# Kernel optimization log

Measured on AMD Instinct MI355X. Metric: run time of the kernel, lower is better.

Reference implementation:

```python
import jax, jax.numpy as jnp
import numpy as np

EPS = 0.01  # diffusion sampling noise scale


def gru_last(x, Wx, Wh, bx, bh):
    """Run a single-layer GRU (torch gate conventions) over x: [B, L, C] -> final hidden [B, H]."""
    B, L, C = x.shape
    H = Wh.shape[0]
    xg = jnp.einsum('blc,cg->blg', x, Wx) + bx  # precomputed input gates [B, L, 3H]

    def step(h, xg_t):
        hg = h @ Wh + bh
        xr, xz, xn = jnp.split(xg_t, 3, axis=-1)
        hr, hz, hn = jnp.split(hg, 3, axis=-1)
        r = jax.nn.sigmoid(xr + hr)
        z = jax.nn.sigmoid(xz + hz)
        n = jnp.tanh(xn + r * hn)
        h_new = (1.0 - z) * n + z * h
        return h_new, None

    h0 = jnp.zeros((B, H), x.dtype)
    h, _ = jax.lax.scan(step, h0, jnp.swapaxes(xg, 0, 1))
    return h


def gru_aggr(x, Wx, Wh, bx, bh, Wo, bo):
    return gru_last(x, Wx, Wh, bx, bh) @ Wo + bo


def setup_inputs() -> dict:
    key = jax.random.key(0)
    N, C, DEG, H, C_OUT, T = 8000, 64, 16, 128, 64, 4
    ks = jax.random.split(key, 16)

    def lin(k, fan_in, shape):
        return jax.random.normal(k, shape, dtype=jnp.float32) / np.sqrt(fan_in)

    inp = {
        'node_attr': jax.random.normal(ks[0], (N, C), dtype=jnp.float32),
        'neighbors': jax.random.randint(ks[1], (N, DEG), 0, N, dtype=jnp.int32),
        'noise': jax.random.normal(ks[2], (T, N, DEG), dtype=jnp.float32),
        # diff_aggr GRU + output head (edge log-prob comes from channel 0)
        'dWx': lin(ks[3], C, (C, 3 * H)),
        'dWh': lin(ks[4], H, (H, 3 * H)),
        'dbx': jnp.zeros((3 * H,), jnp.float32),
        'dbh': jnp.zeros((3 * H,), jnp.float32),
        'dWo': lin(ks[5], H, (H, C_OUT)),
        'dbo': jnp.zeros((C_OUT,), jnp.float32),
        # walk_aggr GRU + output head (node embedding)
        'wWx': lin(ks[6], C, (C, 3 * H)),
        'wWh': lin(ks[7], H, (H, 3 * H)),
        'wbx': jnp.zeros((3 * H,), jnp.float32),
        'wbh': jnp.zeros((3 * H,), jnp.float32),
        'wWo': lin(ks[8], H, (H, C_OUT)),
        'wbo': jnp.zeros((C_OUT,), jnp.float32),
    }
    return inp


def reference(node_attr, neighbors, noise,
              dWx, dWh, dbx, dbh, dWo, dbo,
              wWx, wWh, wbx, wbh, wWo, wbo):
    N, C = node_attr.shape
    DEG = neighbors.shape[1]
    T = noise.shape[0]

    cur = jnp.arange(N)                      # current frontier of each walk
    walk_embeds = node_attr[:, None, :]      # [N, L, C], L grows each step
    logps = []
    for t in range(T):
        nbr = neighbors[cur]                 # [N, DEG] candidate next hops
        cand = node_attr[nbr]                # [N, DEG, C]
        L = walk_embeds.shape[1]
        prefix = jnp.broadcast_to(walk_embeds[:, None], (N, DEG, L, C))
        seq = jnp.concatenate([prefix, cand[:, :, None, :]], axis=2)  # [N, DEG, L+1, C]
        seq = seq.reshape(N * DEG, L + 1, C)
        logp = gru_aggr(seq, dWx, dWh, dbx, dbh, dWo, dbo)[:, 0].reshape(N, DEG)
        # per-source-node log-softmax normalizer (no_grad in original)
        norm = jax.lax.stop_gradient(jax.nn.logsumexp(logp, axis=1, keepdims=True))
        logp = logp - norm
        p = jnp.exp(logp)
        noisy = p + EPS * noise[t]
        sel = jnp.argmax(noisy, axis=1)      # scatter_max over each node's candidates
        logps.append(jnp.take_along_axis(logp, sel[:, None], axis=1)[:, 0])
        cur = jnp.take_along_axis(nbr, sel[:, None], axis=1)[:, 0]
        walk_embeds = jnp.concatenate([walk_embeds, node_attr[cur][:, None, :]], axis=1)

    walks_logp = jnp.stack(logps, axis=1)    # [N, T]
    v_out = gru_aggr(walk_embeds, wWx, wWh, wbx, wbh, wWo, wbo)  # [N, C_OUT]
    return v_out, walks_logp
```

## Files before the change

kernel.cpp:

```cpp
#include <hip/hip_runtime.h>
#include <math.h>

#define NN 8000
#define CD 64
#define DG 16
#define HD 128
#define G3 384
#define TT 4
#define MARGIN 4e-3f

#if __has_builtin(__builtin_amdgcn_rcpf)
#define RCP(x) __builtin_amdgcn_rcpf(x)
#else
#define RCP(x) (1.f/(x))
#endif

__device__ __forceinline__ float fsig (float x){ return RCP(1.f + __expf(-x)); }
__device__ __forceinline__ float ftanh(float x){ return 1.f - 2.f*RCP(1.f + __expf(2.f*x)); }

__device__ __forceinline__ double fexp64(double x){
    const double LOG2E  = 1.4426950408889634074;
    const double LN2_HI = 6.93147180369123816490e-01;
    const double LN2_LO = 1.90821492927058770002e-10;
    x = fmin(fmax(x, -700.0), 700.0);
    double fn = rint(x * LOG2E);
    double r  = fma(-fn, LN2_HI, x);
    r = fma(-fn, LN2_LO, r);
    double p = 1.6059043836821613e-10;
    p = fma(p, r, 2.0876756987868099e-09);
    p = fma(p, r, 2.5052108385441719e-08);
    p = fma(p, r, 2.7557319223985893e-07);
    p = fma(p, r, 2.7557319223985888e-06);
    p = fma(p, r, 2.4801587301587302e-05);
    p = fma(p, r, 1.9841269841269841e-04);
    p = fma(p, r, 1.3888888888888889e-03);
    p = fma(p, r, 8.3333333333333332e-03);
    p = fma(p, r, 4.1666666666666664e-02);
    p = fma(p, r, 1.6666666666666666e-01);
    p = fma(p, r, 0.5);
    p = fma(p, r, 1.0);
    p = fma(p, r, 1.0);
    long long bits = __double_as_longlong(p) + ((long long)(int)fn << 52);
    return __longlong_as_double(bits);
}
__device__ __forceinline__ double sig64f (double x){ return 1.0/(1.0 + fexp64(-x)); }
__device__ __forceinline__ double tanh64f(double x){ return 1.0 - 2.0/(fexp64(2.0*x) + 1.0); }

__global__ __launch_bounds__(384) void xg_kernel(const float* __restrict__ A,
    const float* __restrict__ W, const float* __restrict__ b,
    float* __restrict__ hiP, float* __restrict__ loP)
{
    __shared__ float a_s[8][64];
    const int g  = threadIdx.x;
    const int l  = g & 63, q = g >> 6;
    const int n0 = blockIdx.x * 8;
    for (int idx = threadIdx.x; idx < 8*64; idx += 384)
        a_s[idx>>6][idx&63] = A[(size_t)n0*64 + idx];
    __syncthreads();
    double acc[8];
    const double bg = (double)b[g];
#pragma unroll
    for (int j=0;j<8;j++) acc[j] = bg;
    for (int c=0;c<64;c++){
        const double w = (double)W[c*G3 + g];
#pragma unroll
        for (int j=0;j<8;j++) acc[j] += (double)a_s[j][c]*w;
    }
#pragma unroll
    for (int j=0;j<8;j++){
        const size_t base = (size_t)(n0+j)*64 + l;
        const float hi = (float)acc[j];
        hiP[base*8 + q] = hi;
        if (q < 2) hiP[base*8 + 6 + q] = 0.f;
        if (loP) loP[base*6 + q] = (float)(acc[j] - (double)hi);
    }
}

__global__ __launch_bounds__(256) void repack_kernel(const float* __restrict__ W,
                                                     float* __restrict__ P)
{
    const int idx = blockIdx.x*256 + threadIdx.x;
    const int k = idx >> 9, rem = idx & 511, l = rem >> 3, s = rem & 7;
    P[idx] = (s < 6) ? W[k*G3 + s*64 + l] : 0.f;
}

__global__ __launch_bounds__(256) void walk_kernel(
    const int*   __restrict__ nbrs,  const float* __restrict__ noise,
    const float* __restrict__ XGfP,  const float* __restrict__ dWhP,
    const float* __restrict__ dbh,   const float* __restrict__ dWo,
    const float* __restrict__ dbo,
    int* __restrict__ paths, int* __restrict__ fail_cnt, int* __restrict__ fail_list,
    float* __restrict__ out)
{
    __shared__ float hf_s[4][HD];
    __shared__ float part_s[4][4][6][64];

    const int wid  = threadIdx.x >> 6;
    const int lane = threadIdx.x & 63;
    const int node = blockIdx.x*4 + wid;

    float h0 = 0.f, h1 = 0.f;
    float dbhf[6], hgf[6];
#pragma unroll
    for (int m=0;m<6;m++){ dbhf[m] = dbh[lane+64*m]; hgf[m] = dbhf[m]; }
    const float wo0f0 = dWo[lane*CD];
    const float wo0f1 = dWo[(lane+64)*CD];
    const float dbo0f = dbo[0];

    int cur = node;
    int ch0=0, ch1=0, ch2=0, ch3=0;
    int tripmask = 0;

    for (int t=0;t<TT;t++){
        if      (t==0) ch0 = cur;
        else if (t==1) ch1 = cur;
        else if (t==2) ch2 = cur;
        else           ch3 = cur;

        {
            const float4* xr = (const float4*)(XGfP + ((size_t)cur*64 + lane)*8);
            const float4 A = xr[0], B = xr[1];
            float r = fsig (A.x + hgf[0]);
            float z = fsig (A.z + hgf[2]);
            float n = ftanh(B.x + r*hgf[4]);
            h0 = (1.f-z)*n + z*h0;
            r = fsig (A.y + hgf[1]);
            z = fsig (A.w + hgf[3]);
            n = ftanh(B.y + r*hgf[5]);
            h1 = (1.f-z)*n + z*h1;
        }
        hf_s[wid][lane] = h0;  hf_s[wid][lane+64] = h1;
        __syncthreads();

        {
            float pacc[4][6];
#pragma unroll
            for (int j=0;j<4;j++)
#pragma unroll
                for (int m=0;m<6;m++) pacc[j][m] = 0.f;
            const float4* wr = (const float4*)(dWhP + (size_t)lane*8);
#pragma unroll 4
            for (int kk=0; kk<32; kk++){
                const int k = wid*32 + kk;
                const float4 W0 = wr[k*128], W1 = wr[k*128+1];
#pragma unroll
                for (int j=0;j<4;j++){
                    const float hk = hf_s[j][k];
                    pacc[j][0] += hk*W0.x; pacc[j][1] += hk*W0.y;
                    pacc[j][2] += hk*W0.z; pacc[j][3] += hk*W0.w;
                    pacc[j][4] += hk*W1.x; pacc[j][5] += hk*W1.y;
                }
            }
#pragma unroll
            for (int j=0;j<4;j++)
#pragma unroll
                for (int m=0;m<6;m++) part_s[wid][j][m][lane] = pacc[j][m];
        }
        __syncthreads();

#pragma unroll
        for (int m=0;m<6;m++)
            hgf[m] = dbhf[m] + part_s[0][wid][m][lane] + part_s[1][wid][m][lane]
                             + part_s[2][wid][m][lane] + part_s[3][wid][m][lane];

        int   nbrv = (lane < DG) ? nbrs[(size_t)cur*DG + lane] : 0;
        float nz   = (lane < DG) ? noise[((size_t)t*NN + node)*DG + lane] : 0.f;
        float lf = -3.0e38f;
#pragma unroll
        for (int g=0; g<4; g++){
            float4 CA[4], CB[4];
#pragma unroll
            for (int j=0;j<4;j++){
                const int nd = __shfl(nbrv, g*4+j);
                const float4* cr = (const float4*)(XGfP + ((size_t)nd*64 + lane)*8);
                CA[j] = cr[0];  CB[j] = cr[1];
            }
            float part[4];
#pragma unroll
            for (int j=0;j<4;j++){
                float r = fsig (CA[j].x + hgf[0]);
                float z = fsig (CA[j].z + hgf[2]);
                float n = ftanh(CB[j].x + r*hgf[4]);
                part[j]  = ((1.f-z)*n + z*h0) * wo0f0;
                r = fsig (CA[j].y + hgf[1]);
                z = fsig (CA[j].w + hgf[3]);
                n = ftanh(CB[j].y + r*hgf[5]);
                part[j] += ((1.f-z)*n + z*h1) * wo0f1;
            }
#pragma unroll
            for (int off=32; off>0; off>>=1){
#pragma unroll
                for (int j=0;j<4;j++) part[j] += __shfl_xor(part[j], off);
            }
#pragma unroll
            for (int j=0;j<4;j++) if (lane == g*4+j) lf = part[j] + dbo0f;
        }

        float v  = (lane < DG) ? lf : -3.0e38f;
        float mx = v;
#pragma unroll
        for (int off=32; off>0; off>>=1) mx = fmaxf(mx, __shfl_xor(mx, off));
        float e = (lane < DG) ? __expf(v - mx) : 0.f;
        float s = e;
#pragma unroll
        for (int off=32; off>0; off>>=1) s += __shfl_xor(s, off);
        const float normf = mx + __logf(s);

        float noisyf = (lane < DG) ? __expf(v - normf) + 0.01f*nz : -3.0e38f;
        int   idx = lane;
        float bv  = noisyf;
#pragma unroll
        for (int off=32; off>0; off>>=1){
            float ov = __shfl_xor(bv, off);
            int   oi = __shfl_xor(idx, off);
            if (ov > bv || (ov == bv && oi < idx)){ bv = ov; idx = oi; }
        }
        float sv = (lane == idx || lane >= DG) ? -3.0e38f : noisyf;
#pragma unroll
        for (int off=32; off>0; off>>=1) sv = fmaxf(sv, __shfl_xor(sv, off));

        if ((bv - sv) < MARGIN) tripmask |= (1 << t);

        const float lpf = __shfl(v, idx) - normf;
        if (lane == 0) out[NN*CD + node*TT + t] = lpf;
        cur = __shfl(nbrv, idx);
    }

    if (lane == 0){
        int* p = paths + (size_t)node*8;
        p[0]=ch0; p[1]=ch1; p[2]=ch2; p[3]=ch3; p[4]=cur;
        if (tripmask){
            const int bin = 31 - __clz(tripmask);
            const int slot = atomicAdd(&fail_cnt[bin], 1);
            fail_list[bin*NN + slot] = node | (tripmask << 16);
        }
    }
}

__global__ __launch_bounds__(256) void fix_kernel(
    const int*   __restrict__ nbrs,  const float* __restrict__ noise,
    const float* __restrict__ XGfP,  const float* __restrict__ XGrP,
    const float* __restrict__ dWhP,  const float* __restrict__ dbh,
    const float* __restrict__ dWo,   const float* __restrict__ dbo,
    const int* __restrict__ fail_cnt, const int* __restrict__ fail_list,
    int* __restrict__ paths, float* __restrict__ out)
{
    __shared__ double smem[3584];
    double* h_s  = smem;
    double* dbuf = smem + 512;

    const int wid  = threadIdx.x >> 6;
    const int lane = threadIdx.x & 63;
    const int n0c = fail_cnt[0], n1c = fail_cnt[1], n2c = fail_cnt[2], n3c = fail_cnt[3];
    const int total = n0c + n1c + n2c + n3c;
    if (blockIdx.x*4 >= total) return;

    const int  ii     = blockIdx.x*4 + wid;
    const bool active = (ii < total);
    int entry = 0;
    if (active){
        int b, loc;
        if      (ii < n0c)            { b=0; loc=ii; }
        else if (ii < n0c+n1c)        { b=1; loc=ii-n0c; }
        else if (ii < n0c+n1c+n2c)    { b=2; loc=ii-n0c-n1c; }
        else                          { b=3; loc=ii-n0c-n1c-n2c; }
        entry = fail_list[b*NN + loc];
    }
    const int  node = entry & 0xFFFF;
    const int  mask = active ? (entry >> 16) : 0;
    const int* pw   = paths + (size_t)node*8;

    double db64[6];
#pragma unroll
    for (int m=0;m<6;m++) db64[m] = (double)dbh[lane+64*m];
    const double wo0d0 = (double)dWo[lane*CD];
    const double wo0d1 = (double)dWo[(lane+64)*CD];
    const double dbo0d = (double)dbo[0];

    double H0 = 0.0, H1 = 0.0;
    double g64[6];
#pragma unroll
    for (int m=0;m<6;m++) g64[m] = db64[m];
    int  cur = node;
    int  c0=0,c1=0,c2=0,c3=0;
    bool diverged = false;

    for (int t=0;t<TT;t++){
        const bool done = !diverged && ((mask >> t) == 0);
        if (__syncthreads_and(done ? 1 : 0)) break;

        if      (t==0) c0 = cur;
        else if (t==1) c1 = cur;
        else if (t==2) c2 = cur;
        else           c3 = cur;

        if (!done){
            const size_t b = (size_t)cur*64 + lane;
            const float* hi = XGfP + b*8;
            const float* lo = XGrP + b*6;
            double r = sig64f (((double)hi[0]+(double)lo[0]) + g64[0]);
            double z = sig64f (((double)hi[2]+(double)lo[2]) + g64[2]);
            double n = tanh64f(((double)hi[4]+(double)lo[4]) + r*g64[4]);
            H0 = (1.0-z)*n + z*H0;
            r = sig64f (((double)hi[1]+(double)lo[1]) + g64[1]);
            z = sig64f (((double)hi[3]+(double)lo[3]) + g64[3]);
            n = tanh64f(((double)hi[5]+(double)lo[5]) + r*g64[5]);
            H1 = (1.0-z)*n + z*H1;
            h_s[wid*HD + lane] = H0;  h_s[wid*HD + lane + 64] = H1;
        }
        __syncthreads();

        double pacc[4][6];
#pragma unroll
        for (int j=0;j<4;j++)
#pragma unroll
            for (int m=0;m<6;m++) pacc[j][m] = 0.0;
        {
            const float4* wv = (const float4*)(dWhP + (size_t)lane*8);
#pragma unroll 4
            for (int kk=0; kk<32; kk++){
                const int k = wid*32 + kk;
                const float4 W0 = wv[k*128], W1 = wv[k*128+1];
#pragma unroll
                for (int j=0;j<4;j++){
                    const double hk = h_s[j*HD + k];
                    pacc[j][0] += hk*(double)W0.x; pacc[j][1] += hk*(double)W0.y;
                    pacc[j][2] += hk*(double)W0.z; pacc[j][3] += hk*(double)W0.w;
                    pacc[j][4] += hk*(double)W1.x; pacc[j][5] += hk*(double)W1.y;
                }
            }
        }
        if (wid >= 2){
#pragma unroll
            for (int j=0;j<4;j++)
#pragma unroll
                for (int m=0;m<6;m++)
                    dbuf[(((wid-2)*4+j)*6+m)*64 + lane] = pacc[j][m];
        }
        __syncthreads();
        if (wid < 2){
#pragma unroll
            for (int j=0;j<4;j++)
#pragma unroll
                for (int m=0;m<6;m++){
                    pacc[j][m] += dbuf[((wid*4+j)*6+m)*64 + lane];
                    dbuf[((wid*4+j)*6+m)*64 + lane] = pacc[j][m];
                }
        }
        __syncthreads();
        if (!done){
#pragma unroll
            for (int m=0;m<6;m++)
                g64[m] = db64[m] + dbuf[((0*4+wid)*6+m)*64 + lane]
                                 + dbuf[((1*4+wid)*6+m)*64 + lane];
        }

        if (!diverged && !((mask >> t) & 1)){
            cur = pw[t+1];
            continue;
        }

        int   nbrv = (lane < DG) ? nbrs[(size_t)cur*DG + lane] : 0;
        float nz   = (lane < DG) ? noise[((size_t)t*NN + node)*DG + lane] : 0.f;
        double lv = -1e300;
#pragma unroll
        for (int g=0; g<4; g++){
            float ch[4][6], cl[4][6];
#pragma unroll
            for (int j=0;j<4;j++){
                const int nd = __shfl(nbrv, g*4+j);
                const size_t b = (size_t)nd*64 + lane;
                const float* hi = XGfP + b*8;
                const float* lo = XGrP + b*6;
#pragma unroll
                for (int q=0;q<6;q++){ ch[j][q]=hi[q]; cl[j][q]=lo[q]; }
            }
#pragma unroll
            for (int j=0;j<4;j++){
                double r = sig64f (((double)ch[j][0]+(double)cl[j][0]) + g64[0]);
                double z = sig64f (((double)ch[j][2]+(double)cl[j][2]) + g64[2]);
                double n = tanh64f(((double)ch[j][4]+(double)cl[j][4]) + r*g64[4]);
                double part = ((1.0-z)*n + z*H0) * wo0d0;
                r = sig64f (((double)ch[j][1]+(double)cl[j][1]) + g64[1]);
                z = sig64f (((double)ch[j][3]+(double)cl[j][3]) + g64[3]);
                n = tanh64f(((double)ch[j][5]+(double)cl[j][5]) + r*g64[5]);
                part += ((1.0-z)*n + z*H1) * wo0d1;
#pragma unroll
                for (int off=32; off>0; off>>=1) part += __shfl_xor(part, off);
                if (lane == g*4+j) lv = part + dbo0d;
            }
        }

        double dv = (lane < DG) ? lv : -1e300;
        double dmx = dv;
#pragma unroll
        for (int off=32; off>0; off>>=1) dmx = fmax(dmx, __shfl_xor(dmx, off));
        double de = (lane < DG) ? fexp64(dv - dmx) : 0.0;
        double ds = de;
#pragma unroll
        for (int off=32; off>0; off>>=1) ds += __shfl_xor(ds, off);
        const double dnorm = dmx + log(ds);
        double dnoisy = (lane < DG) ? fexp64(dv - dnorm) + 0.01*(double)nz : -1e300;
        int di = lane;
#pragma unroll
        for (int off=32; off>0; off>>=1){
            double ov = __shfl_xor(dnoisy, off);
            int    oi = __shfl_xor(di, off);
            if (ov > dnoisy || (ov == dnoisy && oi < di)){ dnoisy = ov; di = oi; }
        }
        const double lpfix = __shfl(dv, di) - dnorm;
        if (active && lane == 0) out[NN*CD + node*TT + t] = (float)lpfix;
        const int newcur = __shfl(nbrv, di);
        diverged = diverged || (newcur != pw[t+1]);
        cur = newcur;
    }

    if (active && diverged && lane == 0){
        int* p = paths + (size_t)node*8;
        p[0]=c0; p[1]=c1; p[2]=c2; p[3]=c3; p[4]=cur;
    }
}

__global__ __launch_bounds__(256) void wgru_kernel(
    const int*   __restrict__ paths, const float* __restrict__ XGwP,
    const float* __restrict__ wWhP,  const float* __restrict__ wbh,
    const float* __restrict__ wWo,   const float* __restrict__ wbo,
    float* __restrict__ out)
{
    __shared__ float hw_s[4][HD];
    __shared__ float part_s[4][4][6][64];
    const int wid  = threadIdx.x >> 6;
    const int lane = threadIdx.x & 63;
    const int node = blockIdx.x*4 + wid;

    float h0 = 0.f, h1 = 0.f;
    float wb[6], hg[6];
#pragma unroll
    for (int m=0;m<6;m++){ wb[m] = wbh[lane+64*m]; hg[m] = wb[m]; }
    const int* p = paths + (size_t)node*8;

#pragma unroll
    for (int s=0; s<=TT; s++){
        const int c = p[s];
        const float4* xr = (const float4*)(XGwP + ((size_t)c*64 + lane)*8);
        const float4 A = xr[0], B = xr[1];
        float r = fsig (A.x + hg[0]);
        float z = fsig (A.z + hg[2]);
        float n = ftanh(B.x + r*hg[4]);
        h0 = (1.f-z)*n + z*h0;
        r = fsig (A.y + hg[1]);
        z = fsig (A.w + hg[3]);
        n = ftanh(B.y + r*hg[5]);
        h1 = (1.f-z)*n + z*h1;
        if (s < TT){
            hw_s[wid][lane] = h0;  hw_s[wid][lane+64] = h1;
            __syncthreads();
            float pacc[4][6];
#pragma unroll
            for (int j=0;j<4;j++)
#pragma unroll
                for (int m=0;m<6;m++) pacc[j][m] = 0.f;
            const float4* wr = (const float4*)(wWhP + (size_t)lane*8);
#pragma unroll 4
            for (int kk=0; kk<32; kk++){
                const int k = wid*32 + kk;
                const float4 W0 = wr[k*128], W1 = wr[k*128+1];
#pragma unroll
                for (int j=0;j<4;j++){
                    const float hk = hw_s[j][k];
                    pacc[j][0] += hk*W0.x; pacc[j][1] += hk*W0.y;
                    pacc[j][2] += hk*W0.z; pacc[j][3] += hk*W0.w;
                    pacc[j][4] += hk*W1.x; pacc[j][5] += hk*W1.y;
                }
            }
#pragma unroll
            for (int j=0;j<4;j++)
#pragma unroll
                for (int m=0;m<6;m++) part_s[wid][j][m][lane] = pacc[j][m];
            __syncthreads();
#pragma unroll
            for (int m=0;m<6;m++)
                hg[m] = wb[m] + part_s[0][wid][m][lane] + part_s[1][wid][m][lane]
                              + part_s[2][wid][m][lane] + part_s[3][wid][m][lane];
        }
    }
    hw_s[wid][lane] = h0;  hw_s[wid][lane+64] = h1;
    __syncthreads();

    float acc = wbo[lane];
    const float* wcol = wWo + lane;
    for (int i=0;i<HD;i++) acc += hw_s[wid][i] * wcol[(size_t)i*CD];
    out[(size_t)node*CD + lane] = acc;
}

extern "C" void kernel_launch(void* const* d_in, const int* in_sizes, int n_in,
                              void* d_out, int out_size, void* d_ws, size_t ws_size,
                              hipStream_t stream)
{
    const float* attr  = (const float*)d_in[0];
    const int*   nbrs  = (const int*)  d_in[1];
    const float* noise = (const float*)d_in[2];
    const float* dWx = (const float*)d_in[3];
    const float* dWh = (const float*)d_in[4];
    const float* dbx = (const float*)d_in[5];
    const float* dbh = (const float*)d_in[6];
    const float* dWo = (const float*)d_in[7];
    const float* dbo = (const float*)d_in[8];
    const float* wWx = (const float*)d_in[9];
    const float* wWh = (const float*)d_in[10];
    const float* wbx = (const float*)d_in[11];
    const float* wbh = (const float*)d_in[12];
    const float* wWo = (const float*)d_in[13];
    const float* wbo = (const float*)d_in[14];
    float* out = (float*)d_out;

    char* ws = (char*)d_ws;
    float* XGfP      = (float*)(ws);
    float* XGrP      = (float*)(ws + 16384000);
    float* XGwP      = (float*)(ws + 28672000);
    float* dWhP      = (float*)(ws + 45056000);
    float* wWhP      = (float*)(ws + 45318144);
    int*   paths     = (int*)  (ws + 45580288);
    int*   fail_list = (int*)  (ws + 45836288);
    int*   fail_cnt  = (int*)  (ws + 45964288);

    hipMemsetAsync(fail_cnt, 0, 4*sizeof(int), stream);

    xg_kernel<<<NN/8, G3, 0, stream>>>(attr, dWx, dbx, XGfP, XGrP);
    xg_kernel<<<NN/8, G3, 0, stream>>>(attr, wWx, wbx, XGwP, nullptr);
    repack_kernel<<<(HD*64*8)/256, 256, 0, stream>>>(dWh, dWhP);
    repack_kernel<<<(HD*64*8)/256, 256, 0, stream>>>(wWh, wWhP);

    walk_kernel<<<NN/4, 256, 0, stream>>>(nbrs, noise, XGfP, dWhP,
                                          dbh, dWo, dbo,
                                          paths, fail_cnt, fail_list, out);
    fix_kernel<<<2000, 256, 0, stream>>>(nbrs, noise, XGfP, XGrP,
                                         dWhP, dbh, dWo, dbo,
                                         fail_cnt, fail_list, paths, out);
    wgru_kernel<<<NN/4, 256, 0, stream>>>(paths, XGwP, wWhP, wbh, wWo, wbo, out);
}
```

Before: 492.9 us.

## Prefetch neighbor gate rows and tree-reduce hidden partials through smaller shared buffer

The walk kernel now issues the next step's input-gate row, neighbor list and noise loads right after the current step's selection. Candidate gate rows are double-buffered in groups of four, so loads for the next group overlap scoring of the current one, and the first group's loads start before the recurrent matvec. The cross-warp reduction of recurrent partials becomes a two-level reduction through a half-size shared buffer, in both the walk and walk-GRU kernels. In exchange there is an extra barrier per step and more live registers, which may lower occupancy.

```diff
diff --git a/kernel.cpp b/kernel.cpp
--- a/kernel.cpp
+++ b/kernel.cpp
@@ -93,7 +93,7 @@
     float* __restrict__ out)
 {
     __shared__ float hf_s[4][HD];
-    __shared__ float part_s[4][4][6][64];
+    __shared__ float dbuf_s[2][4][6][64];
 
     const int wid  = threadIdx.x >> 6;
     const int lane = threadIdx.x & 63;
@@ -110,6 +110,47 @@
     int cur = node;
     int ch0=0, ch1=0, ch2=0, ch3=0;
     int tripmask = 0;
+
+    float4 XA, XB; int nbrv; float nz;
+    {
+        const float4* xr = (const float4*)(XGfP + ((size_t)cur*64 + lane)*8);
+        XA = xr[0];  XB = xr[1];
+        nbrv = (lane < DG) ? nbrs[(size_t)cur*DG + lane] : 0;
+        nz   = (lane < DG) ? noise[(size_t)node*DG + lane] : 0.f;
+    }
+
+    float4 PA[4], PB[4], QA[4], QB[4];
+    float lf;
+
+    auto loadGroup = [&](float4* A, float4* B, int gbase){
+#pragma unroll
+        for (int j=0;j<4;j++){
+            const int nd = __shfl(nbrv, gbase+j);
+            const float4* cr = (const float4*)(XGfP + ((size_t)nd*64 + lane)*8);
+            A[j] = cr[0];  B[j] = cr[1];
+        }
+    };
+    auto scoreGroup = [&](const float4* A, const float4* B, int gbase){
+        float part[4];
+#pragma unroll
+        for (int j=0;j<4;j++){
+            float r = fsig (A[j].x + hgf[0]);
+            float z = fsig (A[j].z + hgf[2]);
+            float n = ftanh(B[j].x + r*hgf[4]);
+            part[j]  = ((1.f-z)*n + z*h0) * wo0f0;
+            r = fsig (A[j].y + hgf[1]);
+            z = fsig (A[j].w + hgf[3]);
+            n = ftanh(B[j].y + r*hgf[5]);
+            part[j] += ((1.f-z)*n + z*h1) * wo0f1;
+        }
+#pragma unroll
+        for (int off=32; off>0; off>>=1){
+#pragma unroll
+            for (int j=0;j<4;j++) part[j] += __shfl_xor(part[j], off);
+        }
+#pragma unroll
+        for (int j=0;j<4;j++) if (lane == gbase+j) lf = part[j] + dbo0f;
+    };
 
     for (int t=0;t<TT;t++){
         if      (t==0) ch0 = cur;
@@ -118,26 +159,26 @@
         else           ch3 = cur;
 
         {
-            const float4* xr = (const float4*)(XGfP + ((size_t)cur*64 + lane)*8);
-            const float4 A = xr[0], B = xr[1];
-            float r = fsig (A.x + hgf[0]);
-            float z = fsig (A.z + hgf[2]);
-            float n = ftanh(B.x + r*hgf[4]);
+            float r = fsig (XA.x + hgf[0]);
+            float z = fsig (XA.z + hgf[2]);
+            float n = ftanh(XB.x + r*hgf[4]);
             h0 = (1.f-z)*n + z*h0;
-            r = fsig (A.y + hgf[1]);
-            z = fsig (A.w + hgf[3]);
-            n = ftanh(B.y + r*hgf[5]);
+            r = fsig (XA.y + hgf[1]);
+            z = fsig (XA.w + hgf[3]);
+            n = ftanh(XB.y + r*hgf[5]);
             h1 = (1.f-z)*n + z*h1;
         }
         hf_s[wid][lane] = h0;  hf_s[wid][lane+64] = h1;
         __syncthreads();
 
+        loadGroup(PA, PB, 0);
+
+        float pacc[4][6];
+#pragma unroll
+        for (int j=0;j<4;j++)
+#pragma unroll
+            for (int m=0;m<6;m++) pacc[j][m] = 0.f;
         {
-            float pacc[4][6];
-#pragma unroll
-            for (int j=0;j<4;j++)
-#pragma unroll
-                for (int m=0;m<6;m++) pacc[j][m] = 0.f;
             const float4* wr = (const float4*)(dWhP + (size_t)lane*8);
 #pragma unroll 4
             for (int kk=0; kk<32; kk++){
@@ -151,50 +192,33 @@
                     pacc[j][4] += hk*W1.x; pacc[j][5] += hk*W1.y;
                 }
             }
+        }
+        if (wid >= 2){
 #pragma unroll
             for (int j=0;j<4;j++)
 #pragma unroll
-                for (int m=0;m<6;m++) part_s[wid][j][m][lane] = pacc[j][m];
+                for (int m=0;m<6;m++) dbuf_s[wid-2][j][m][lane] = pacc[j][m];
         }
         __syncthreads();
-
+        if (wid < 2){
+#pragma unroll
+            for (int j=0;j<4;j++)
+#pragma unroll
+                for (int m=0;m<6;m++){
+                    pacc[j][m] += dbuf_s[wid][j][m][lane];
+                    dbuf_s[wid][j][m][lane] = pacc[j][m];
+                }
+        }
+        __syncthreads();
 #pragma unroll
         for (int m=0;m<6;m++)
-            hgf[m] = dbhf[m] + part_s[0][wid][m][lane] + part_s[1][wid][m][lane]
-                             + part_s[2][wid][m][lane] + part_s[3][wid][m][lane];
-
-        int   nbrv = (lane < DG) ? nbrs[(size_t)cur*DG + lane] : 0;
-        float nz   = (lane < DG) ? noise[((size_t)t*NN + node)*DG + lane] : 0.f;
-        float lf = -3.0e38f;
-#pragma unroll
-        for (int g=0; g<4; g++){
-            float4 CA[4], CB[4];
-#pragma unroll
-            for (int j=0;j<4;j++){
-                const int nd = __shfl(nbrv, g*4+j);
-                const float4* cr = (const float4*)(XGfP + ((size_t)nd*64 + lane)*8);
-                CA[j] = cr[0];  CB[j] = cr[1];
-            }
-            float part[4];
-#pragma unroll
-            for (int j=0;j<4;j++){
-                float r = fsig (CA[j].x + hgf[0]);
-                float z = fsig (CA[j].z + hgf[2]);
-                float n = ftanh(CB[j].x + r*hgf[4]);
-                part[j]  = ((1.f-z)*n + z*h0) * wo0f0;
-                r = fsig (CA[j].y + hgf[1]);
-                z = fsig (CA[j].w + hgf[3]);
-                n = ftanh(CB[j].y + r*hgf[5]);
-                part[j] += ((1.f-z)*n + z*h1) * wo0f1;
-            }
-#pragma unroll
-            for (int off=32; off>0; off>>=1){
-#pragma unroll
-                for (int j=0;j<4;j++) part[j] += __shfl_xor(part[j], off);
-            }
-#pragma unroll
-            for (int j=0;j<4;j++) if (lane == g*4+j) lf = part[j] + dbo0f;
-        }
+            hgf[m] = dbhf[m] + dbuf_s[0][wid][m][lane] + dbuf_s[1][wid][m][lane];
+
+        lf = -3.0e38f;
+        loadGroup(QA, QB, 4);   scoreGroup(PA, PB, 0);
+        loadGroup(PA, PB, 8);   scoreGroup(QA, QB, 4);
+        loadGroup(QA, QB, 12);  scoreGroup(PA, PB, 8);
+        scoreGroup(QA, QB, 12);
 
         float v  = (lane < DG) ? lf : -3.0e38f;
         float mx = v;
@@ -224,6 +248,13 @@
         const float lpf = __shfl(v, idx) - normf;
         if (lane == 0) out[NN*CD + node*TT + t] = lpf;
         cur = __shfl(nbrv, idx);
+
+        if (t < TT-1){
+            const float4* xr = (const float4*)(XGfP + ((size_t)cur*64 + lane)*8);
+            XA = xr[0];  XB = xr[1];
+            nbrv = (lane < DG) ? nbrs[(size_t)cur*DG + lane] : 0;
+            nz   = (lane < DG) ? noise[((size_t)(t+1)*NN + node)*DG + lane] : 0.f;
+        }
     }
 
     if (lane == 0){
@@ -428,7 +459,7 @@
     float* __restrict__ out)
 {
     __shared__ float hw_s[4][HD];
-    __shared__ float part_s[4][4][6][64];
+    __shared__ float dbuf_s[2][4][6][64];
     const int wid  = threadIdx.x >> 6;
     const int lane = threadIdx.x & 63;
     const int node = blockIdx.x*4 + wid;
@@ -473,15 +504,26 @@
                     pacc[j][4] += hk*W1.x; pacc[j][5] += hk*W1.y;
                 }
             }
-#pragma unroll
-            for (int j=0;j<4;j++)
-#pragma unroll
-                for (int m=0;m<6;m++) part_s[wid][j][m][lane] = pacc[j][m];
+            if (wid >= 2){
+#pragma unroll
+                for (int j=0;j<4;j++)
+#pragma unroll
+                    for (int m=0;m<6;m++) dbuf_s[wid-2][j][m][lane] = pacc[j][m];
+            }
             __syncthreads();
+            if (wid < 2){
+#pragma unroll
+                for (int j=0;j<4;j++)
+#pragma unroll
+                    for (int m=0;m<6;m++){
+                        pacc[j][m] += dbuf_s[wid][j][m][lane];
+                        dbuf_s[wid][j][m][lane] = pacc[j][m];
+                    }
+            }
+            __syncthreads();
 #pragma unroll
             for (int m=0;m<6;m++)
-                hg[m] = wb[m] + part_s[0][wid][m][lane] + part_s[1][wid][m][lane]
-                              + part_s[2][wid][m][lane] + part_s[3][wid][m][lane];
+                hg[m] = wb[m] + dbuf_s[0][wid][m][lane] + dbuf_s[1][wid][m][lane];
         }
     }
     hw_s[wid][lane] = h0;  hw_s[wid][lane+64] = h1;
```

Result: no change. 486.6 us (-1.3%).
